# Optimization experiments

Hardware: AMD Instinct MI355X
Metric: run time of the kernel (lower is better)

## Reference

```python
import jax, jax.numpy as jnp
import numpy as np

D = 96           # fine dense grid edge
SF = 2           # scale_factor
S = SF ** 3      # sub-voxels per coarse voxel
DS = D // SF     # coarse grid edge
C = 64           # in_channels
OUT = 64         # out_channels


def setup_inputs() -> dict:
    key = jax.random.key(0)
    k1, k2 = jax.random.split(key)
    N = D ** 3
    # dense grid ijk in canonical (lexicographic) order -> sorted in_index holds
    r = jnp.arange(N, dtype=jnp.int32)
    ijk = jnp.stack([r // (D * D), (r // D) % D, r % D], axis=-1)  # [N,3] int32
    in_data = jax.random.normal(k1, (N, C), dtype=jnp.float32)
    w_out = jax.random.normal(k2, (S * C, OUT), dtype=jnp.float32) * (1.0 / np.sqrt(S * C))
    return {"in_data": in_data, "ijk": ijk, "w_out": w_out}


def reference(in_data, ijk, w_out):
    ijk = ijk.astype(jnp.int32)
    down_ijk = ijk // SF                      # floor division (coords >= 0)
    local = ijk - down_ijk * SF               # [N,3] in [0, SF)
    # local flat index: i*SF^2 + j*SF + k
    local_index = local[:, 0] * (SF * SF) + local[:, 1] * SF + local[:, 2]
    # canonical index into dense coarsened grid (matches ijk_to_index on dense grid)
    down_index = down_ijk[:, 0] * (DS * DS) + down_ijk[:, 1] * DS + down_ijk[:, 2]
    flat_idx = down_index * S + local_index    # [N], unique by construction
    # scatter_add into pre-zeroed buffer (space-to-depth reorg)
    flat_target = jnp.zeros((DS ** 3 * S, C), dtype=in_data.dtype)
    flat_target = flat_target.at[flat_idx].add(in_data)
    down_data = flat_target.reshape(DS ** 3, S * C)   # [Nd, S*C]
    out = down_data @ w_out                            # [Nd, OUT]
    return out
```

## Files before the change

kernel.cpp:

```cpp
#include <hip/hip_runtime.h>
#include <hip/hip_bf16.h>

#define DD 96
#define DSS 48
#define CCH 64
#define OUTC 64

typedef __bf16 bf16_t;
typedef __bf16 bf16x8 __attribute__((ext_vector_type(8)));
typedef float f32x4 __attribute__((ext_vector_type(4)));
typedef unsigned int u32;
typedef unsigned short u16;

__device__ __forceinline__ u16 f2bf(float f) {
    u32 u = __builtin_bit_cast(u32, f);
    u += 0x7FFFu + ((u >> 16) & 1u);
    return (u16)(u >> 16);
}

__global__ void wprep_kernel(const float* __restrict__ w, u16* __restrict__ wf) {
    int id = blockIdx.x * 256 + threadIdx.x;
    if (id >= 16 * 64 * 8 * 4) return;
    int j  = id & 7;
    int L  = (id >> 3) & 63;
    int ks = (id >> 9) & 15;
    int t  = id >> 13;
    int k  = ks * 32 + (L >> 4) * 8 + j;
    int n  = t * 16 + (L & 15);
    wf[id] = f2bf(w[k * OUTC + n]);
}

template <bool USE_WS>
__global__ __launch_bounds__(192) void ds_gemm_kernel(
    const float* __restrict__ in,
    const float* __restrict__ w,
    const u16* __restrict__ wf,
    float* __restrict__ out)
{
    const int tid  = threadIdx.x;
    const int wv   = tid >> 6;
    const int lane = tid & 63;
    const int q    = lane >> 4;
    const int mrow = lane & 15;
    const int b    = blockIdx.x;
    const int di   = b / DSS;
    const int dj   = b % DSS;
    const int dkb  = wv * 16;

    const float* base[4];
#pragma unroll
    for (int c = 0; c < 4; c++) {
        const int li = c >> 1, lj = c & 1;
        base[c] = in + (size_t)((2 * di + li) * (DD * DD) + (2 * dj + lj) * DD) * CCH;
    }
    const int laneoff = 2 * (dkb + mrow) * CCH + q * 8;

    auto aaddr = [&](int ks) -> const f32x4* {
        return (const f32x4*)(base[ks >> 2] + laneoff
                              + ((ks >> 1) & 1) * CCH + (ks & 1) * 32);
    };
    auto bload = [&](int ks, int nt) -> bf16x8 {
        bf16x8 t;
        if (USE_WS) {
            __builtin_memcpy(&t, wf + (size_t)(((nt * 16 + ks) * 64) + lane) * 8, 16);
        } else {
            union { bf16x8 v; u16 s[8]; } u2;
#pragma unroll
            for (int j = 0; j < 8; j++)
                u2.s[j] = f2bf(w[(ks * 32 + q * 8 + j) * OUTC + nt * 16 + mrow]);
            t = u2.v;
        }
        return t;
    };

    f32x4 acc[4];
#pragma unroll
    for (int nt = 0; nt < 4; nt++) acc[nt] = f32x4{0.f, 0.f, 0.f, 0.f};

    f32x4 ar0 = aaddr(0)[0];
    f32x4 ar1 = aaddr(0)[1];
    bf16x8 bcur[4];
#pragma unroll
    for (int nt = 0; nt < 4; nt++) bcur[nt] = bload(0, nt);

#pragma unroll
    for (int ks = 0; ks < 16; ks++) {
        f32x4 nr0, nr1;
        bf16x8 bnext[4];
        if (ks < 15) {
            nr0 = aaddr(ks + 1)[0];
            nr1 = aaddr(ks + 1)[1];
#pragma unroll
            for (int nt = 0; nt < 4; nt++) bnext[nt] = bload(ks + 1, nt);
        }
        union { bf16x8 v; bf16_t e[8]; } af;
        af.e[0] = (bf16_t)ar0.x; af.e[1] = (bf16_t)ar0.y;
        af.e[2] = (bf16_t)ar0.z; af.e[3] = (bf16_t)ar0.w;
        af.e[4] = (bf16_t)ar1.x; af.e[5] = (bf16_t)ar1.y;
        af.e[6] = (bf16_t)ar1.z; af.e[7] = (bf16_t)ar1.w;
#pragma unroll
        for (int nt = 0; nt < 4; nt++)
            acc[nt] = __builtin_amdgcn_mfma_f32_16x16x32_bf16(af.v, bcur[nt], acc[nt], 0, 0, 0);
        if (ks < 15) {
            ar0 = nr0; ar1 = nr1;
#pragma unroll
            for (int nt = 0; nt < 4; nt++) bcur[nt] = bnext[nt];
        }
    }

    const int mb = b * 48 + dkb + q * 4;
#pragma unroll
    for (int nt = 0; nt < 4; nt++)
#pragma unroll
        for (int r = 0; r < 4; r++)
            out[(size_t)(mb + r) * OUTC + nt * 16 + mrow] = acc[nt][r];
}

extern "C" void kernel_launch(void* const* d_in, const int* in_sizes, int n_in,
                              void* d_out, int out_size, void* d_ws, size_t ws_size,
                              hipStream_t stream) {
    const float* in = (const float*)d_in[0];
    const float* w  = (const float*)d_in[2];
    float* out = (float*)d_out;

    if (ws_size >= 65536) {
        wprep_kernel<<<128, 256, 0, stream>>>(w, (u16*)d_ws);
        ds_gemm_kernel<true><<<DSS * DSS, 192, 0, stream>>>(
            in, w, (const u16*)d_ws, out);
    } else {
        ds_gemm_kernel<false><<<DSS * DSS, 192, 0, stream>>>(in, w, nullptr, out);
    }
}
```

Baseline: 331.1 us.

## Process two M-tiles per wave to reuse B fragments across MFMAs

Each wave now computes two 16-row output tiles, which may come from different coarse columns, sharing the same B fragments per k-step. Blocks grow to four waves and the grid shrinks to cover the same tile count. This halves weight-fragment loads per output and doubles in-flight A loads per wave. The cost is higher register pressure and fewer total waves, which may reduce latency hiding for the memory-bound input stream.

Measured after the change: 342.6 us. 3.5% more time.

```diff
diff --git a/kernel.cpp b/kernel.cpp
--- a/kernel.cpp
+++ b/kernel.cpp
@@ -31,7 +31,7 @@
 }
 
 template <bool USE_WS>
-__global__ __launch_bounds__(192) void ds_gemm_kernel(
+__global__ __launch_bounds__(256) void ds_gemm_kernel(
     const float* __restrict__ in,
     const float* __restrict__ w,
     const u16* __restrict__ wf,
@@ -42,27 +42,36 @@
     const int lane = tid & 63;
     const int q    = lane >> 4;
     const int mrow = lane & 15;
-    const int b    = blockIdx.x;
-    const int di   = b / DSS;
-    const int dj   = b % DSS;
-    const int dkb  = wv * 16;
 
-    const float* base[4];
+    const int t0 = (blockIdx.x * 4 + wv) * 2;
+
+    const float* base[2][4];
+    int dkoff[2];
+    int mb[2];
 #pragma unroll
-    for (int c = 0; c < 4; c++) {
-        const int li = c >> 1, lj = c & 1;
-        base[c] = in + (size_t)((2 * di + li) * (DD * DD) + (2 * dj + lj) * DD) * CCH;
+    for (int i = 0; i < 2; i++) {
+        const int t   = t0 + i;
+        const int col = t / 3;
+        const int seg = t - col * 3;
+        const int di  = col / DSS;
+        const int dj  = col - di * DSS;
+#pragma unroll
+        for (int c = 0; c < 4; c++) {
+            const int li = c >> 1, lj = c & 1;
+            base[i][c] = in + (size_t)((2 * di + li) * (DD * DD) + (2 * dj + lj) * DD) * CCH;
+        }
+        dkoff[i] = 2 * (seg * 16 + mrow) * CCH + q * 8;
+        mb[i]    = col * 48 + seg * 16 + q * 4;
     }
-    const int laneoff = 2 * (dkb + mrow) * CCH + q * 8;
 
-    auto aaddr = [&](int ks) -> const f32x4* {
-        return (const f32x4*)(base[ks >> 2] + laneoff
+    auto aaddr = [&](int i, int ks) -> const f32x4* {
+        return (const f32x4*)(base[i][ks >> 2] + dkoff[i]
                               + ((ks >> 1) & 1) * CCH + (ks & 1) * 32);
     };
     auto bload = [&](int ks, int nt) -> bf16x8 {
         bf16x8 t;
         if (USE_WS) {
-            __builtin_memcpy(&t, wf + (size_t)(((nt * 16 + ks) * 64) + lane) * 8, 16);
+            __builtin_memcpy(&t, wf + (size_t)((nt * 16 + ks) * 64 + lane) * 8, 16);
         } else {
             union { bf16x8 v; u16 s[8]; } u2;
 #pragma unroll
@@ -73,47 +82,62 @@
         return t;
     };
 
-    f32x4 acc[4];
+    f32x4 acc[2][4];
 #pragma unroll
-    for (int nt = 0; nt < 4; nt++) acc[nt] = f32x4{0.f, 0.f, 0.f, 0.f};
+    for (int i = 0; i < 2; i++)
+#pragma unroll
+        for (int nt = 0; nt < 4; nt++) acc[i][nt] = f32x4{0.f, 0.f, 0.f, 0.f};
 
-    f32x4 ar0 = aaddr(0)[0];
-    f32x4 ar1 = aaddr(0)[1];
-    bf16x8 bcur[4];
+    f32x4 ar[2][2];
+    bf16x8 bc[4];
 #pragma unroll
-    for (int nt = 0; nt < 4; nt++) bcur[nt] = bload(0, nt);
+    for (int i = 0; i < 2; i++) { ar[i][0] = aaddr(i, 0)[0]; ar[i][1] = aaddr(i, 0)[1]; }
+#pragma unroll
+    for (int nt = 0; nt < 4; nt++) bc[nt] = bload(0, nt);
 
 #pragma unroll
     for (int ks = 0; ks < 16; ks++) {
-        f32x4 nr0, nr1;
-        bf16x8 bnext[4];
+        f32x4 nr[2][2];
+        bf16x8 bn[4];
         if (ks < 15) {
-            nr0 = aaddr(ks + 1)[0];
-            nr1 = aaddr(ks + 1)[1];
 #pragma unroll
-            for (int nt = 0; nt < 4; nt++) bnext[nt] = bload(ks + 1, nt);
+            for (int i = 0; i < 2; i++) {
+                nr[i][0] = aaddr(i, ks + 1)[0];
+                nr[i][1] = aaddr(i, ks + 1)[1];
+            }
+#pragma unroll
+            for (int nt = 0; nt < 4; nt++) bn[nt] = bload(ks + 1, nt);
         }
-        union { bf16x8 v; bf16_t e[8]; } af;
-        af.e[0] = (bf16_t)ar0.x; af.e[1] = (bf16_t)ar0.y;
-        af.e[2] = (bf16_t)ar0.z; af.e[3] = (bf16_t)ar0.w;
-        af.e[4] = (bf16_t)ar1.x; af.e[5] = (bf16_t)ar1.y;
-        af.e[6] = (bf16_t)ar1.z; af.e[7] = (bf16_t)ar1.w;
+        bf16x8 af[2];
+#pragma unroll
+        for (int i = 0; i < 2; i++) {
+            union { bf16x8 v; bf16_t e[8]; } u2;
+            u2.e[0] = (bf16_t)ar[i][0].x; u2.e[1] = (bf16_t)ar[i][0].y;
+            u2.e[2] = (bf16_t)ar[i][0].z; u2.e[3] = (bf16_t)ar[i][0].w;
+            u2.e[4] = (bf16_t)ar[i][1].x; u2.e[5] = (bf16_t)ar[i][1].y;
+            u2.e[6] = (bf16_t)ar[i][1].z; u2.e[7] = (bf16_t)ar[i][1].w;
+            af[i] = u2.v;
+        }
 #pragma unroll
         for (int nt = 0; nt < 4; nt++)
-            acc[nt] = __builtin_amdgcn_mfma_f32_16x16x32_bf16(af.v, bcur[nt], acc[nt], 0, 0, 0);
+#pragma unroll
+            for (int i = 0; i < 2; i++)
+                acc[i][nt] = __builtin_amdgcn_mfma_f32_16x16x32_bf16(af[i], bc[nt], acc[i][nt], 0, 0, 0);
         if (ks < 15) {
-            ar0 = nr0; ar1 = nr1;
 #pragma unroll
-            for (int nt = 0; nt < 4; nt++) bcur[nt] = bnext[nt];
+            for (int i = 0; i < 2; i++) { ar[i][0] = nr[i][0]; ar[i][1] = nr[i][1]; }
+#pragma unroll
+            for (int nt = 0; nt < 4; nt++) bc[nt] = bn[nt];
         }
     }
 
-    const int mb = b * 48 + dkb + q * 4;
 #pragma unroll
-    for (int nt = 0; nt < 4; nt++)
+    for (int i = 0; i < 2; i++)
 #pragma unroll
-        for (int r = 0; r < 4; r++)
-            out[(size_t)(mb + r) * OUTC + nt * 16 + mrow] = acc[nt][r];
+        for (int nt = 0; nt < 4; nt++)
+#pragma unroll
+            for (int r = 0; r < 4; r++)
+                out[(size_t)(mb[i] + r) * OUTC + nt * 16 + mrow] = acc[i][nt][r];
 }
 
 extern "C" void kernel_launch(void* const* d_in, const int* in_sizes, int n_in,
@@ -125,9 +149,9 @@
 
     if (ws_size >= 65536) {
         wprep_kernel<<<128, 256, 0, stream>>>(w, (u16*)d_ws);
-        ds_gemm_kernel<true><<<DSS * DSS, 192, 0, stream>>>(
+        ds_gemm_kernel<true><<<864, 256, 0, stream>>>(
             in, w, (const u16*)d_ws, out);
     } else {
-        ds_gemm_kernel<false><<<DSS * DSS, 192, 0, stream>>>(in, w, nullptr, out);
+        ds_gemm_kernel<false><<<864, 256, 0, stream>>>(in, w, nullptr, out);
     }
 }
```
